# Kernel tuning notes

Measured on AMD Instinct MI355X. Metric: run time of the kernel, lower is better.

Reference implementation:

```python
import jax, jax.numpy as jnp
import numpy as np


def _pairwise_sq_dist_mean(x):
    """Mean over feature dim of pairwise squared distances: D[i,j] = mean_k (x[j,k]-x[i,k])^2.
    Uses the ||a||^2 + ||b||^2 - 2ab identity instead of the O(n^2*d) broadcast."""
    d = x.shape[1]
    sq = jnp.sum(x * x, axis=1)  # [n]
    gram = x @ x.T               # [n, n]
    return (sq[:, None] + sq[None, :] - 2.0 * gram) / d


def setup_inputs() -> dict:
    key = jax.random.key(0)
    k1, k2 = jax.random.split(key)
    noises = jax.random.normal(k1, (4096, 256), dtype=jnp.float32)
    images = jax.random.normal(k2, (4096, 3, 64, 64), dtype=jnp.float32)
    return {"noises": noises, "images": images}


def reference(noises, images):
    if images.ndim > 2:
        images = images.reshape(images.shape[0], -1)
    images_dist = _pairwise_sq_dist_mean(images)  # [B, B]
    noises_dist = _pairwise_sq_dist_mean(noises)  # [B, B]
    return jnp.exp(jnp.mean(-images_dist * noises_dist))
```

## Files before the change

### kernel.cpp

```cpp
#include <hip/hip_runtime.h>
#include <stdint.h>
#include <math.h>

typedef __attribute__((ext_vector_type(8))) short short8;
typedef __attribute__((ext_vector_type(4))) float f32x4;

typedef __attribute__((address_space(1))) const uint32_t g_u32;
typedef __attribute__((address_space(3))) uint32_t l_u32;

static __device__ __forceinline__ uint16_t f2bf(float f) {
  union { float f; uint32_t u; } v; v.f = f;
  uint32_t r = (v.u + 0x7FFFu + ((v.u >> 16) & 1u)) >> 16;
  return (uint16_t)r;
}

static __device__ __forceinline__ float waveReduceSum(float x) {
#pragma unroll
  for (int m = 32; m > 0; m >>= 1) x += __shfl_xor(x, m, 64);
  return x;
}

__global__ __launch_bounds__(256) void k_noise_b(const float* __restrict__ N,
                                                 float* __restrict__ b) {
  const int wave = threadIdx.x >> 6, lane = threadIdx.x & 63;
  const int i = blockIdx.x * 4 + wave;
  const float4 v = *reinterpret_cast<const float4*>(N + (size_t)i * 256 + lane * 4);
  float s = v.x * v.x + v.y * v.y + v.z * v.z + v.w * v.w;
  s = waveReduceSum(s);
  if (lane == 0) b[i] = s;
}

__global__ __launch_bounds__(256) void k_nt(const float* __restrict__ N,
                                            uint16_t* __restrict__ Nt) {
  __shared__ __align__(16) uint16_t T[256 * 72];
  const int i0 = blockIdx.x * 64;
  const int tid = threadIdx.x;
#pragma unroll
  for (int it = 0; it < 16; ++it) {
    const int k = (tid >> 6) + it * 4;
    const int l4 = (tid & 63) * 4;
    const float4 v = *reinterpret_cast<const float4*>(N + (size_t)(i0 + k) * 256 + l4);
    T[(l4 + 0) * 72 + k] = f2bf(v.x);
    T[(l4 + 1) * 72 + k] = f2bf(v.y);
    T[(l4 + 2) * 72 + k] = f2bf(v.z);
    T[(l4 + 3) * 72 + k] = f2bf(v.w);
  }
  __syncthreads();
  const int l = tid;
#pragma unroll
  for (int tt = 0; tt < 2; ++tt) {
    const int tg = blockIdx.x * 2 + tt;
#pragma unroll
    for (int c = 0; c < 4; ++c) {
      const short8 v = *reinterpret_cast<const short8*>(&T[l * 72 + tt * 32 + c * 8]);
      *reinterpret_cast<short8*>((char*)Nt + (size_t)tg * 16384 + l * 64 +
                                 ((c ^ (l & 3)) << 4)) = v;
    }
  }
}

__global__ __launch_bounds__(256) void k_x_pass(const float* __restrict__ X,
                                                const float* __restrict__ b,
                                                float* __restrict__ a,
                                                float* __restrict__ sx,
                                                float* __restrict__ cx, int D1) {
  const int ncb = D1 >> 10;
  const int colblk = blockIdx.x % ncb;
  const int rowblk = blockIdx.x / ncb;
  const int wv = threadIdx.x >> 6, lane = threadIdx.x & 63;
  const int col = (colblk << 10) + (wv << 8) + (lane << 2);
  const int row0 = rowblk << 6;
  float s0 = 0.f, s1 = 0.f, s2 = 0.f, s3 = 0.f;
  float c0 = 0.f, c1 = 0.f, c2 = 0.f, c3 = 0.f;
  const float* p = X + (size_t)row0 * D1 + col;
  for (int r8 = 0; r8 < 64; r8 += 8) {
    float asq[8];
#pragma unroll
    for (int r = 0; r < 8; ++r) {
      const float4 v = *reinterpret_cast<const float4*>(p + (size_t)(r8 + r) * D1);
      const float bi = b[row0 + r8 + r];
      s0 += v.x; s1 += v.y; s2 += v.z; s3 += v.w;
      c0 += bi * v.x; c1 += bi * v.y; c2 += bi * v.z; c3 += bi * v.w;
      asq[r] = v.x * v.x + v.y * v.y + v.z * v.z + v.w * v.w;
    }
#pragma unroll
    for (int m = 1; m < 64; m <<= 1) {
#pragma unroll
      for (int r = 0; r < 8; ++r) asq[r] += __shfl_xor(asq[r], m, 64);
    }
    float myv = asq[0];
#pragma unroll
    for (int r = 1; r < 8; ++r) myv = (lane == r) ? asq[r] : myv;
    if (lane < 8) atomicAdd(&a[row0 + r8 + lane], myv);
  }
  atomicAdd(&sx[col + 0], s0); atomicAdd(&sx[col + 1], s1);
  atomicAdd(&sx[col + 2], s2); atomicAdd(&sx[col + 3], s3);
  atomicAdd(&cx[col + 0], c0); atomicAdd(&cx[col + 1], c1);
  atomicAdd(&cx[col + 2], c2); atomicAdd(&cx[col + 3], c3);
}

__global__ __launch_bounds__(256) void k_noise2(const float* __restrict__ N,
                                                const float* __restrict__ a,
                                                float* __restrict__ sn,
                                                float* __restrict__ an) {
  const int t = threadIdx.x;
  const int i0 = blockIdx.x << 6;
  float ssn = 0.f, san = 0.f;
  for (int r = 0; r < 64; ++r) {
    const int i = i0 + r;
    const float v = N[(size_t)i * 256 + t];
    ssn += v;
    san += a[i] * v;
  }
  atomicAdd(&sn[t], ssn);
  atomicAdd(&an[t], san);
}

__global__ __launch_bounds__(256, 3) void k_gemm_f2(const float* __restrict__ X,
                                                    const uint16_t* __restrict__ Nt,
                                                    float* __restrict__ M,
                                                    int B, int D1) {
  __shared__ __align__(16) uint16_t NB[2][8192];
  __shared__ __align__(16) uint16_t AB[2][64 * 40];
  const int tid = threadIdx.x;
  const int w = tid >> 6, lane = tid & 63;
  const int lr = lane & 15, lh = lane >> 4;
  const int nks = B >> 7;
  const int pt = blockIdx.x >> 2, kc = blockIdx.x & 3;
  const int pbase = pt << 6;
  const int ks0 = kc * nks;

  f32x4 acc[4][4];
#pragma unroll
  for (int i = 0; i < 4; ++i)
#pragma unroll
    for (int j = 0; j < 4; ++j) acc[i][j] = (f32x4){0.f, 0.f, 0.f, 0.f};

  const int ap = tid & 63, ak8 = (tid >> 6) << 3;
  const float* Xbase = X + (size_t)(ks0 * 32 + ak8) * D1 + pbase + ap;
  float xr[8];

#define GLL_B(S, BUF)                                                              \
  {                                                                                \
    const char* gsrc_ = (const char*)Nt + (size_t)(ks0 + (S)) * 16384 +            \
                        ((size_t)w << 10) + (size_t)lane * 16;                     \
    _Pragma("unroll")                                                              \
    for (int j_ = 0; j_ < 4; ++j_) {                                               \
      __builtin_amdgcn_global_load_lds((g_u32*)(gsrc_ + ((size_t)j_ << 12)),       \
                                       (l_u32*)&NB[BUF][(j_ * 4 + w) << 9],        \
                                       16, 0, 0);                                  \
    }                                                                              \
  }
#define A_LOADS(S)                                                                 \
  {                                                                                \
    const float* p_ = Xbase + (size_t)(S) * 32 * D1;                               \
    _Pragma("unroll")                                                              \
    for (int r_ = 0; r_ < 8; ++r_) xr[r_] = p_[(size_t)r_ * D1];                   \
  }

  GLL_B(0, 0);
  A_LOADS(0);

  for (int s = 0; s < nks; ++s) {
    const int buf = s & 1;
    {
      union { uint16_t u[8]; short8 v; } pk;
#pragma unroll
      for (int r = 0; r < 8; ++r) pk.u[r] = f2bf(xr[r]);
      *reinterpret_cast<short8*>(&AB[buf][ap * 40 + ak8]) = pk.v;
    }
    __syncthreads();
    if (s + 1 < nks) {
      GLL_B(s + 1, buf ^ 1);
      A_LOADS(s + 1);
    }
    short8 af[4], bfv[4];
#pragma unroll
    for (int ps = 0; ps < 4; ++ps)
      af[ps] = *reinterpret_cast<const short8*>(&AB[buf][(ps * 16 + lr) * 40 + lh * 8]);
#pragma unroll
    for (int q = 0; q < 4; ++q) {
      const int l = (w << 6) + (q << 4) + lr;
      bfv[q] = *reinterpret_cast<const short8*>(&NB[buf][l * 32 + ((lh ^ (l & 3)) << 3)]);
    }
#pragma unroll
    for (int ps = 0; ps < 4; ++ps)
#pragma unroll
      for (int q = 0; q < 4; ++q)
        acc[ps][q] = __builtin_amdgcn_mfma_f32_16x16x32_bf16(af[ps], bfv[q], acc[ps][q], 0, 0, 0);
    __syncthreads();
  }
#undef GLL_B
#undef A_LOADS

#pragma unroll
  for (int ps = 0; ps < 4; ++ps)
#pragma unroll
    for (int q = 0; q < 4; ++q)
#pragma unroll
      for (int e = 0; e < 4; ++e) {
        const int p = pbase + ps * 16 + lh * 4 + e;
        const int l = (w << 6) + (q << 4) + lr;
        atomicAdd(&M[(size_t)p * 256 + l], acc[ps][q][e]);
      }
}

__global__ __launch_bounds__(256) void k_square(const float* __restrict__ M,
                                                float* __restrict__ Fp, int nf4) {
  __shared__ float red[4];
  float s = 0.f;
  for (int idx = blockIdx.x * 256 + threadIdx.x; idx < nf4; idx += gridDim.x * 256) {
    const float4 v = reinterpret_cast<const float4*>(M)[idx];
    s += v.x * v.x + v.y * v.y + v.z * v.z + v.w * v.w;
  }
  s = waveReduceSum(s);
  const int wave = threadIdx.x >> 6, lane = threadIdx.x & 63;
  if (lane == 0) red[wave] = s;
  __syncthreads();
  if (threadIdx.x == 0) atomicAdd(Fp, red[0] + red[1] + red[2] + red[3]);
}

__global__ __launch_bounds__(256) void k_gemm_f(const float* __restrict__ X,
                                                const float* __restrict__ Nz,
                                                float* __restrict__ Fout,
                                                int B, int D1) {
  __shared__ uint16_t Abf[64 * 40];
  __shared__ uint16_t Bbf[256 * 40];
  __shared__ float red[4];
  const int tid = threadIdx.x;
  const int pbase = blockIdx.x << 6;
  const int wave = tid >> 6, lane = tid & 63;
  const int lr = lane & 15, lh = lane >> 4;

  f32x4 acc[4][4];
#pragma unroll
  for (int i = 0; i < 4; ++i)
#pragma unroll
    for (int j = 0; j < 4; ++j) acc[i][j] = (f32x4){0.f, 0.f, 0.f, 0.f};

  const int igx = tid & 7, p4x = ((tid >> 3) & 15) << 2;
  const int ign0 = tid & 7, l4n0 = (tid >> 3) << 2;
  const int ign1 = (tid + 256) & 7, l4n1 = ((tid + 256) >> 3) << 2;

  float4 xr0, xr1, xr2, xr3;
  float4 n0r0, n0r1, n0r2, n0r3;
  float4 n1r0, n1r1, n1r2, n1r3;

  auto load_stage = [&](int i0) {
    if (tid < 128) {
      const float* src = X + (size_t)(i0 + igx * 4) * D1 + pbase + p4x;
      xr0 = *reinterpret_cast<const float4*>(src);
      xr1 = *reinterpret_cast<const float4*>(src + D1);
      xr2 = *reinterpret_cast<const float4*>(src + 2 * (size_t)D1);
      xr3 = *reinterpret_cast<const float4*>(src + 3 * (size_t)D1);
    }
    {
      const float* src = Nz + (size_t)(i0 + ign0 * 4) * 256 + l4n0;
      n0r0 = *reinterpret_cast<const float4*>(src);
      n0r1 = *reinterpret_cast<const float4*>(src + 256);
      n0r2 = *reinterpret_cast<const float4*>(src + 512);
      n0r3 = *reinterpret_cast<const float4*>(src + 768);
    }
    {
      const float* src = Nz + (size_t)(i0 + ign1 * 4) * 256 + l4n1;
      n1r0 = *reinterpret_cast<const float4*>(src);
      n1r1 = *reinterpret_cast<const float4*>(src + 256);
      n1r2 = *reinterpret_cast<const float4*>(src + 512);
      n1r3 = *reinterpret_cast<const float4*>(src + 768);
    }
  };

  auto store_stage = [&]() {
    ushort4 w;
    if (tid < 128) {
      w.x = f2bf(xr0.x); w.y = f2bf(xr1.x); w.z = f2bf(xr2.x); w.w = f2bf(xr3.x);
      *reinterpret_cast<ushort4*>(&Abf[(p4x + 0) * 40 + igx * 4]) = w;
      w.x = f2bf(xr0.y); w.y = f2bf(xr1.y); w.z = f2bf(xr2.y); w.w = f2bf(xr3.y);
      *reinterpret_cast<ushort4*>(&Abf[(p4x + 1) * 40 + igx * 4]) = w;
      w.x = f2bf(xr0.z); w.y = f2bf(xr1.z); w.z = f2bf(xr2.z); w.w = f2bf(xr3.z);
      *reinterpret_cast<ushort4*>(&Abf[(p4x + 2) * 40 + igx * 4]) = w;
      w.x = f2bf(xr0.w); w.y = f2bf(xr1.w); w.z = f2bf(xr2.w); w.w = f2bf(xr3.w);
      *reinterpret_cast<ushort4*>(&Abf[(p4x + 3) * 40 + igx * 4]) = w;
    }
    w.x = f2bf(n0r0.x); w.y = f2bf(n0r1.x); w.z = f2bf(n0r2.x); w.w = f2bf(n0r3.x);
    *reinterpret_cast<ushort4*>(&Bbf[(l4n0 + 0) * 40 + ign0 * 4]) = w;
    w.x = f2bf(n0r0.y); w.y = f2bf(n0r1.y); w.z = f2bf(n0r2.y); w.w = f2bf(n0r3.y);
    *reinterpret_cast<ushort4*>(&Bbf[(l4n0 + 1) * 40 + ign0 * 4]) = w;
    w.x = f2bf(n0r0.z); w.y = f2bf(n0r1.z); w.z = f2bf(n0r2.z); w.w = f2bf(n0r3.z);
    *reinterpret_cast<ushort4*>(&Bbf[(l4n0 + 2) * 40 + ign0 * 4]) = w;
    w.x = f2bf(n0r0.w); w.y = f2bf(n0r1.w); w.z = f2bf(n0r2.w); w.w = f2bf(n0r3.w);
    *reinterpret_cast<ushort4*>(&Bbf[(l4n0 + 3) * 40 + ign0 * 4]) = w;

    w.x = f2bf(n1r0.x); w.y = f2bf(n1r1.x); w.z = f2bf(n1r2.x); w.w = f2bf(n1r3.x);
    *reinterpret_cast<ushort4*>(&Bbf[(l4n1 + 0) * 40 + ign1 * 4]) = w;
    w.x = f2bf(n1r0.y); w.y = f2bf(n1r1.y); w.z = f2bf(n1r2.y); w.w = f2bf(n1r3.y);
    *reinterpret_cast<ushort4*>(&Bbf[(l4n1 + 1) * 40 + ign1 * 4]) = w;
    w.x = f2bf(n1r0.z); w.y = f2bf(n1r1.z); w.z = f2bf(n1r2.z); w.w = f2bf(n1r3.z);
    *reinterpret_cast<ushort4*>(&Bbf[(l4n1 + 2) * 40 + ign1 * 4]) = w;
    w.x = f2bf(n1r0.w); w.y = f2bf(n1r1.w); w.z = f2bf(n1r2.w); w.w = f2bf(n1r3.w);
    *reinterpret_cast<ushort4*>(&Bbf[(l4n1 + 3) * 40 + ign1 * 4]) = w;
  };

  load_stage(0);
  for (int i0 = 0; i0 < B; i0 += 32) {
    store_stage();
    __syncthreads();
    if (i0 + 32 < B) load_stage(i0 + 32);

    short8 af[4], bfv[4];
#pragma unroll
    for (int ps = 0; ps < 4; ++ps)
      af[ps] = *reinterpret_cast<const short8*>(&Abf[(ps * 16 + lr) * 40 + lh * 8]);
#pragma unroll
    for (int q = 0; q < 4; ++q)
      bfv[q] = *reinterpret_cast<const short8*>(&Bbf[((wave * 4 + q) * 16 + lr) * 40 + lh * 8]);
#pragma unroll
    for (int ps = 0; ps < 4; ++ps)
#pragma unroll
      for (int q = 0; q < 4; ++q)
        acc[ps][q] = __builtin_amdgcn_mfma_f32_16x16x32_bf16(af[ps], bfv[q], acc[ps][q], 0, 0, 0);
    __syncthreads();
  }

  float loc = 0.f;
#pragma unroll
  for (int ps = 0; ps < 4; ++ps)
#pragma unroll
    for (int q = 0; q < 4; ++q)
#pragma unroll
      for (int e = 0; e < 4; ++e) loc += acc[ps][q][e] * acc[ps][q][e];
  loc = waveReduceSum(loc);
  if (lane == 0) red[wave] = loc;
  __syncthreads();
  if (tid == 0) atomicAdd(Fout, red[0] + red[1] + red[2] + red[3]);
}

__global__ __launch_bounds__(256) void k_final(const float* __restrict__ a,
                                               const float* __restrict__ b,
                                               const float* __restrict__ sx,
                                               const float* __restrict__ cx,
                                               const float* __restrict__ sn,
                                               const float* __restrict__ an,
                                               const float* __restrict__ Fp,
                                               float* __restrict__ out, int B, int D1) {
  const int tid = threadIdx.x;
  float sa = 0.f, sb = 0.f, sab = 0.f, t2 = 0.f;
  for (int i = tid; i < B; i += 256) {
    const float ai = a[i], bi = b[i];
    sa += ai; sb += bi; sab += ai * bi;
  }
  float t1 = an[tid] * sn[tid];
  for (int k = tid; k < D1; k += 256) t2 += cx[k] * sx[k];

  sa = waveReduceSum(sa); sb = waveReduceSum(sb); sab = waveReduceSum(sab);
  t1 = waveReduceSum(t1); t2 = waveReduceSum(t2);
  __shared__ float R[5][4];
  const int wave = tid >> 6, lane = tid & 63;
  if (lane == 0) { R[0][wave] = sa; R[1][wave] = sb; R[2][wave] = sab; R[3][wave] = t1; R[4][wave] = t2; }
  __syncthreads();
  if (tid == 0) {
    double Sa = 0, Sb = 0, Sab = 0, T1 = 0, T2 = 0;
    for (int w = 0; w < 4; ++w) {
      Sa += R[0][w]; Sb += R[1][w]; Sab += R[2][w]; T1 += R[3][w]; T2 += R[4][w];
    }
    const double F = (double)Fp[0];
    const double total = 2.0 * (double)B * Sab + 2.0 * Sa * Sb - 4.0 * T1 - 4.0 * T2 + 4.0 * F;
    const double denom = (double)D1 * 256.0 * (double)B * (double)B;
    out[0] = (float)exp(-total / denom);
  }
}

extern "C" void kernel_launch(void* const* d_in, const int* in_sizes, int n_in,
                              void* d_out, int out_size, void* d_ws, size_t ws_size,
                              hipStream_t stream) {
  const float* noises = (const float*)d_in[0];
  const float* images = (const float*)d_in[1];
  const int B = in_sizes[0] / 256;
  const int D1 = in_sizes[1] / B;

  float* ws = (float*)d_ws;
  float* a  = ws;
  float* b  = ws + B;
  float* sx = ws + 2 * B;
  float* cx = ws + 2 * B + D1;
  float* sn = ws + 2 * B + 2 * D1;
  float* an = ws + 2 * B + 2 * D1 + 256;
  float* Fp = ws + 2 * B + 2 * D1 + 512;
  const size_t m_off = 36864;
  float* M  = ws + m_off;
  uint16_t* Nt = (uint16_t*)(ws + m_off + (size_t)D1 * 256);
  float* outf = (float*)d_out;

  const size_t need = (m_off + (size_t)D1 * 256) * sizeof(float) + (size_t)B * 256 * 2;
  const bool big = ws_size >= need;

  if (big) {
    hipMemsetAsync(d_ws, 0, (m_off + (size_t)D1 * 256) * sizeof(float), stream);
    k_noise_b<<<B / 4, 256, 0, stream>>>(noises, b);
    k_nt<<<B / 64, 256, 0, stream>>>(noises, Nt);
    k_x_pass<<<(D1 / 1024) * (B / 64), 256, 0, stream>>>(images, b, a, sx, cx, D1);
    k_noise2<<<B / 64, 256, 0, stream>>>(noises, a, sn, an);
    k_gemm_f2<<<(D1 / 64) * 4, 256, 0, stream>>>(images, Nt, M, B, D1);
    k_square<<<512, 256, 0, stream>>>(M, Fp, D1 * 256 / 4);
    k_final<<<1, 256, 0, stream>>>(a, b, sx, cx, sn, an, Fp, outf, B, D1);
  } else {
    hipMemsetAsync(d_ws, 0, (size_t)(2 * B + 2 * D1 + 513) * sizeof(float), stream);
    k_noise_b<<<B / 4, 256, 0, stream>>>(noises, b);
    k_x_pass<<<(D1 / 1024) * (B / 64), 256, 0, stream>>>(images, b, a, sx, cx, D1);
    k_noise2<<<B / 64, 256, 0, stream>>>(noises, a, sn, an);
    k_gemm_f<<<D1 / 64, 256, 0, stream>>>(images, noises, Fp, B, D1);
    k_final<<<1, 256, 0, stream>>>(a, b, sx, cx, sn, an, Fp, outf, B, D1);
  }
}
```

Before: 177.7 us.

## Fuse image statistics pass into GEMM and store split-K partials as bf16

Drops the separate image-statistics kernel (k_x_pass) and computes the per-column sums, b-weighted sums and the scalar reductions inside the GEMM's A-tile load loop. The noise norms and column sums move into the transpose kernel, and a new small kernel computes h1. Each of the four split-K slices now writes its partial M in bf16 to its own buffer instead of using fp32 atomicAdds, and the square kernel adds the four slices before squaring. The large memset is replaced by a small zero kernel over the accumulators only. This removes a full extra read of the 200MB image tensor and the atomic traffic, at the cost of bf16 rounding on the partial products and more workspace.

```diff
diff --git a/kernel.cpp b/kernel.cpp
--- a/kernel.cpp
+++ b/kernel.cpp
@@ -14,10 +14,258 @@
   return (uint16_t)r;
 }
 
+static __device__ __forceinline__ float bf2f(uint16_t u) {
+  union { uint32_t u; float f; } v; v.u = ((uint32_t)u) << 16;
+  return v.f;
+}
+
 static __device__ __forceinline__ float waveReduceSum(float x) {
 #pragma unroll
   for (int m = 32; m > 0; m >>= 1) x += __shfl_xor(x, m, 64);
   return x;
+}
+
+__global__ __launch_bounds__(256) void k_zero(float* __restrict__ p, int n4) {
+  const int i = blockIdx.x * 256 + threadIdx.x;
+  if (i < n4) reinterpret_cast<float4*>(p)[i] = float4{0.f, 0.f, 0.f, 0.f};
+}
+
+__global__ __launch_bounds__(256) void k_nt(const float* __restrict__ N,
+                                            uint16_t* __restrict__ Nt,
+                                            float* __restrict__ b,
+                                            float* __restrict__ sn) {
+  __shared__ __align__(16) uint16_t T[256 * 72];
+  const int i0 = blockIdx.x * 64;
+  const int tid = threadIdx.x;
+  const int wave = tid >> 6, lane = tid & 63;
+  float sq[16];
+  float snacc0 = 0.f, snacc1 = 0.f, snacc2 = 0.f, snacc3 = 0.f;
+#pragma unroll
+  for (int it = 0; it < 16; ++it) {
+    const int k = wave + it * 4;
+    const int l4 = lane * 4;
+    const float4 v = *reinterpret_cast<const float4*>(N + (size_t)(i0 + k) * 256 + l4);
+    T[(l4 + 0) * 72 + k] = f2bf(v.x);
+    T[(l4 + 1) * 72 + k] = f2bf(v.y);
+    T[(l4 + 2) * 72 + k] = f2bf(v.z);
+    T[(l4 + 3) * 72 + k] = f2bf(v.w);
+    sq[it] = v.x * v.x + v.y * v.y + v.z * v.z + v.w * v.w;
+    snacc0 += v.x; snacc1 += v.y; snacc2 += v.z; snacc3 += v.w;
+  }
+#pragma unroll
+  for (int m = 1; m < 64; m <<= 1) {
+#pragma unroll
+    for (int it = 0; it < 16; ++it) sq[it] += __shfl_xor(sq[it], m, 64);
+  }
+  float myv = sq[0];
+#pragma unroll
+  for (int it = 1; it < 16; ++it) myv = (lane == it) ? sq[it] : myv;
+  if (lane < 16) b[i0 + wave + lane * 4] = myv;
+  {
+    const int l4 = lane * 4;
+    atomicAdd(&sn[l4 + 0], snacc0); atomicAdd(&sn[l4 + 1], snacc1);
+    atomicAdd(&sn[l4 + 2], snacc2); atomicAdd(&sn[l4 + 3], snacc3);
+  }
+  __syncthreads();
+  const int l = tid;
+#pragma unroll
+  for (int tt = 0; tt < 2; ++tt) {
+    const int tg = blockIdx.x * 2 + tt;
+#pragma unroll
+    for (int c = 0; c < 4; ++c) {
+      const short8 v = *reinterpret_cast<const short8*>(&T[l * 72 + tt * 32 + c * 8]);
+      *reinterpret_cast<short8*>((char*)Nt + (size_t)tg * 16384 + l * 64 +
+                                 ((c ^ (l & 3)) << 4)) = v;
+    }
+  }
+}
+
+__global__ __launch_bounds__(256) void k_h1(const float* __restrict__ N,
+                                            const float* __restrict__ sn,
+                                            float* __restrict__ h1) {
+  const int wave = threadIdx.x >> 6, lane = threadIdx.x & 63;
+  const int i = blockIdx.x * 4 + wave;
+  const float4 v = *reinterpret_cast<const float4*>(N + (size_t)i * 256 + lane * 4);
+  const float4 s = *reinterpret_cast<const float4*>(sn + lane * 4);
+  float d = v.x * s.x + v.y * s.y + v.z * s.z + v.w * s.w;
+  d = waveReduceSum(d);
+  if (lane == 0) h1[i] = d;
+}
+
+__global__ __launch_bounds__(256, 3) void k_gemm_f3(const float* __restrict__ X,
+                                                    const uint16_t* __restrict__ Nt,
+                                                    uint16_t* __restrict__ Mb,
+                                                    const float* __restrict__ bvec,
+                                                    const float* __restrict__ h1v,
+                                                    float* __restrict__ sx,
+                                                    float* __restrict__ cx,
+                                                    float* __restrict__ scal,
+                                                    int B, int D1) {
+  __shared__ __align__(16) uint16_t NB[2][8192];
+  __shared__ __align__(16) uint16_t AB[2][64 * 40];
+  __shared__ float SR[3][4];
+  const int tid = threadIdx.x;
+  const int w = tid >> 6, lane = tid & 63;
+  const int lr = lane & 15, lh = lane >> 4;
+  const int nks = B >> 7;
+  const int pt = blockIdx.x >> 2, kc = blockIdx.x & 3;
+  const int pbase = pt << 6;
+  const int ks0 = kc * nks;
+
+  f32x4 acc[4][4];
+#pragma unroll
+  for (int i = 0; i < 4; ++i)
+#pragma unroll
+    for (int j = 0; j < 4; ++j) acc[i][j] = (f32x4){0.f, 0.f, 0.f, 0.f};
+
+  const int ap = tid & 63, ak8 = (tid >> 6) << 3;
+  const float* Xbase = X + (size_t)(ks0 * 32 + ak8) * D1 + pbase + ap;
+  float xr[8];
+  float4 bv0, bv1, hv0, hv1;
+  float s1 = 0.f, sb = 0.f, sh = 0.f, sxa = 0.f, cxa = 0.f;
+
+#define GLL_B(S, BUF)                                                              \
+  {                                                                                \
+    const char* gsrc_ = (const char*)Nt + (size_t)(ks0 + (S)) * 16384 +            \
+                        ((size_t)w << 10) + (size_t)lane * 16;                     \
+    _Pragma("unroll")                                                              \
+    for (int j_ = 0; j_ < 4; ++j_) {                                               \
+      __builtin_amdgcn_global_load_lds((g_u32*)(gsrc_ + ((size_t)j_ << 12)),       \
+                                       (l_u32*)&NB[BUF][(j_ * 4 + w) << 9],        \
+                                       16, 0, 0);                                  \
+    }                                                                              \
+  }
+#define A_LOADS(S)                                                                 \
+  {                                                                                \
+    const float* p_ = Xbase + (size_t)(S) * 32 * D1;                               \
+    _Pragma("unroll")                                                              \
+    for (int r_ = 0; r_ < 8; ++r_) xr[r_] = p_[(size_t)r_ * D1];                   \
+    const int ib_ = ks0 * 32 + (S) * 32 + ak8;                                     \
+    bv0 = *reinterpret_cast<const float4*>(bvec + ib_);                            \
+    bv1 = *reinterpret_cast<const float4*>(bvec + ib_ + 4);                        \
+    hv0 = *reinterpret_cast<const float4*>(h1v + ib_);                             \
+    hv1 = *reinterpret_cast<const float4*>(h1v + ib_ + 4);                         \
+  }
+
+  GLL_B(0, 0);
+  A_LOADS(0);
+
+  for (int s = 0; s < nks; ++s) {
+    const int buf = s & 1;
+    {
+      union { uint16_t u[8]; short8 v; } pk;
+      const float bb[8] = {bv0.x, bv0.y, bv0.z, bv0.w, bv1.x, bv1.y, bv1.z, bv1.w};
+      const float hh[8] = {hv0.x, hv0.y, hv0.z, hv0.w, hv1.x, hv1.y, hv1.z, hv1.w};
+#pragma unroll
+      for (int r = 0; r < 8; ++r) {
+        const float x = xr[r];
+        pk.u[r] = f2bf(x);
+        const float x2 = x * x;
+        s1 += x2;
+        sb += bb[r] * x2;
+        sh += hh[r] * x2;
+        sxa += x;
+        cxa += bb[r] * x;
+      }
+      *reinterpret_cast<short8*>(&AB[buf][ap * 40 + ak8]) = pk.v;
+    }
+    __syncthreads();
+    if (s + 1 < nks) {
+      GLL_B(s + 1, buf ^ 1);
+      A_LOADS(s + 1);
+    }
+    short8 af[4], bfv[4];
+#pragma unroll
+    for (int ps = 0; ps < 4; ++ps)
+      af[ps] = *reinterpret_cast<const short8*>(&AB[buf][(ps * 16 + lr) * 40 + lh * 8]);
+#pragma unroll
+    for (int q = 0; q < 4; ++q) {
+      const int l = (w << 6) + (q << 4) + lr;
+      bfv[q] = *reinterpret_cast<const short8*>(&NB[buf][l * 32 + ((lh ^ (l & 3)) << 3)]);
+    }
+#pragma unroll
+    for (int ps = 0; ps < 4; ++ps)
+#pragma unroll
+      for (int q = 0; q < 4; ++q)
+        acc[ps][q] = __builtin_amdgcn_mfma_f32_16x16x32_bf16(af[ps], bfv[q], acc[ps][q], 0, 0, 0);
+    __syncthreads();
+  }
+#undef GLL_B
+#undef A_LOADS
+
+  uint16_t* Mk = Mb + (size_t)kc * ((size_t)D1 * 256);
+#pragma unroll
+  for (int ps = 0; ps < 4; ++ps)
+#pragma unroll
+    for (int q = 0; q < 4; ++q) {
+      const int l = (w << 6) + (q << 4) + lr;
+      const int p0 = pbase + ps * 16 + lh * 4;
+      ushort4 st;
+      st.x = f2bf(acc[ps][q][0]); st.y = f2bf(acc[ps][q][1]);
+      st.z = f2bf(acc[ps][q][2]); st.w = f2bf(acc[ps][q][3]);
+      *reinterpret_cast<ushort4*>(&Mk[(size_t)l * D1 + p0]) = st;
+    }
+
+  atomicAdd(&sx[pbase + ap], sxa);
+  atomicAdd(&cx[pbase + ap], cxa);
+
+  s1 = waveReduceSum(s1); sb = waveReduceSum(sb); sh = waveReduceSum(sh);
+  if (lane == 0) { SR[0][w] = s1; SR[1][w] = sb; SR[2][w] = sh; }
+  __syncthreads();
+  if (tid == 0) {
+    atomicAdd(&scal[0], SR[0][0] + SR[0][1] + SR[0][2] + SR[0][3]);
+    atomicAdd(&scal[1], SR[1][0] + SR[1][1] + SR[1][2] + SR[1][3]);
+    atomicAdd(&scal[2], SR[2][0] + SR[2][1] + SR[2][2] + SR[2][3]);
+  }
+}
+
+__global__ __launch_bounds__(256) void k_square(const uint16_t* __restrict__ Mb,
+                                                float* __restrict__ Fp,
+                                                int n8, int slice) {
+  __shared__ float red[4];
+  float s = 0.f;
+  for (int idx = blockIdx.x * 256 + threadIdx.x; idx < n8; idx += gridDim.x * 256) {
+    union { short8 v; uint16_t u[8]; } m0, m1, m2, m3;
+    m0.v = *reinterpret_cast<const short8*>(Mb + (size_t)idx * 8);
+    m1.v = *reinterpret_cast<const short8*>(Mb + (size_t)idx * 8 + (size_t)slice);
+    m2.v = *reinterpret_cast<const short8*>(Mb + (size_t)idx * 8 + 2 * (size_t)slice);
+    m3.v = *reinterpret_cast<const short8*>(Mb + (size_t)idx * 8 + 3 * (size_t)slice);
+#pragma unroll
+    for (int e = 0; e < 8; ++e) {
+      const float v = bf2f(m0.u[e]) + bf2f(m1.u[e]) + bf2f(m2.u[e]) + bf2f(m3.u[e]);
+      s += v * v;
+    }
+  }
+  s = waveReduceSum(s);
+  const int wave = threadIdx.x >> 6, lane = threadIdx.x & 63;
+  if (lane == 0) red[wave] = s;
+  __syncthreads();
+  if (threadIdx.x == 0) atomicAdd(Fp, red[0] + red[1] + red[2] + red[3]);
+}
+
+__global__ __launch_bounds__(256) void k_final3(const float* __restrict__ scal,
+                                                const float* __restrict__ b,
+                                                const float* __restrict__ sx,
+                                                const float* __restrict__ cx,
+                                                float* __restrict__ out,
+                                                int B, int D1) {
+  const int tid = threadIdx.x;
+  float sb_ = 0.f, t2_ = 0.f;
+  for (int i = tid; i < B; i += 256) sb_ += b[i];
+  for (int k = tid; k < D1; k += 256) t2_ += sx[k] * cx[k];
+  sb_ = waveReduceSum(sb_); t2_ = waveReduceSum(t2_);
+  __shared__ float R[2][4];
+  const int wave = tid >> 6, lane = tid & 63;
+  if (lane == 0) { R[0][wave] = sb_; R[1][wave] = t2_; }
+  __syncthreads();
+  if (tid == 0) {
+    double Sb = 0, T2 = 0;
+    for (int w = 0; w < 4; ++w) { Sb += R[0][w]; T2 += R[1][w]; }
+    const double Sa = scal[0], Sab = scal[1], T1 = scal[2], F = scal[3];
+    const double total = 2.0 * (double)B * Sab + 2.0 * Sa * Sb - 4.0 * T1 - 4.0 * T2 + 4.0 * F;
+    const double denom = (double)D1 * 256.0 * (double)B * (double)B;
+    out[0] = (float)exp(-total / denom);
+  }
 }
 
 __global__ __launch_bounds__(256) void k_noise_b(const float* __restrict__ N,
@@ -28,35 +276,6 @@
   float s = v.x * v.x + v.y * v.y + v.z * v.z + v.w * v.w;
   s = waveReduceSum(s);
   if (lane == 0) b[i] = s;
-}
-
-__global__ __launch_bounds__(256) void k_nt(const float* __restrict__ N,
-                                            uint16_t* __restrict__ Nt) {
-  __shared__ __align__(16) uint16_t T[256 * 72];
-  const int i0 = blockIdx.x * 64;
-  const int tid = threadIdx.x;
-#pragma unroll
-  for (int it = 0; it < 16; ++it) {
-    const int k = (tid >> 6) + it * 4;
-    const int l4 = (tid & 63) * 4;
-    const float4 v = *reinterpret_cast<const float4*>(N + (size_t)(i0 + k) * 256 + l4);
-    T[(l4 + 0) * 72 + k] = f2bf(v.x);
-    T[(l4 + 1) * 72 + k] = f2bf(v.y);
-    T[(l4 + 2) * 72 + k] = f2bf(v.z);
-    T[(l4 + 3) * 72 + k] = f2bf(v.w);
-  }
-  __syncthreads();
-  const int l = tid;
-#pragma unroll
-  for (int tt = 0; tt < 2; ++tt) {
-    const int tg = blockIdx.x * 2 + tt;
-#pragma unroll
-    for (int c = 0; c < 4; ++c) {
-      const short8 v = *reinterpret_cast<const short8*>(&T[l * 72 + tt * 32 + c * 8]);
-      *reinterpret_cast<short8*>((char*)Nt + (size_t)tg * 16384 + l * 64 +
-                                 ((c ^ (l & 3)) << 4)) = v;
-    }
-  }
 }
 
 __global__ __launch_bounds__(256) void k_x_pass(const float* __restrict__ X,
@@ -116,110 +335,6 @@
   atomicAdd(&an[t], san);
 }
 
-__global__ __launch_bounds__(256, 3) void k_gemm_f2(const float* __restrict__ X,
-                                                    const uint16_t* __restrict__ Nt,
-                                                    float* __restrict__ M,
-                                                    int B, int D1) {
-  __shared__ __align__(16) uint16_t NB[2][8192];
-  __shared__ __align__(16) uint16_t AB[2][64 * 40];
-  const int tid = threadIdx.x;
-  const int w = tid >> 6, lane = tid & 63;
-  const int lr = lane & 15, lh = lane >> 4;
-  const int nks = B >> 7;
-  const int pt = blockIdx.x >> 2, kc = blockIdx.x & 3;
-  const int pbase = pt << 6;
-  const int ks0 = kc * nks;
-
-  f32x4 acc[4][4];
-#pragma unroll
-  for (int i = 0; i < 4; ++i)
-#pragma unroll
-    for (int j = 0; j < 4; ++j) acc[i][j] = (f32x4){0.f, 0.f, 0.f, 0.f};
-
-  const int ap = tid & 63, ak8 = (tid >> 6) << 3;
-  const float* Xbase = X + (size_t)(ks0 * 32 + ak8) * D1 + pbase + ap;
-  float xr[8];
-
-#define GLL_B(S, BUF)                                                              \
-  {                                                                                \
-    const char* gsrc_ = (const char*)Nt + (size_t)(ks0 + (S)) * 16384 +            \
-                        ((size_t)w << 10) + (size_t)lane * 16;                     \
-    _Pragma("unroll")                                                              \
-    for (int j_ = 0; j_ < 4; ++j_) {                                               \
-      __builtin_amdgcn_global_load_lds((g_u32*)(gsrc_ + ((size_t)j_ << 12)),       \
-                                       (l_u32*)&NB[BUF][(j_ * 4 + w) << 9],        \
-                                       16, 0, 0);                                  \
-    }                                                                              \
-  }
-#define A_LOADS(S)                                                                 \
-  {                                                                                \
-    const float* p_ = Xbase + (size_t)(S) * 32 * D1;                               \
-    _Pragma("unroll")                                                              \
-    for (int r_ = 0; r_ < 8; ++r_) xr[r_] = p_[(size_t)r_ * D1];                   \
-  }
-
-  GLL_B(0, 0);
-  A_LOADS(0);
-
-  for (int s = 0; s < nks; ++s) {
-    const int buf = s & 1;
-    {
-      union { uint16_t u[8]; short8 v; } pk;
-#pragma unroll
-      for (int r = 0; r < 8; ++r) pk.u[r] = f2bf(xr[r]);
-      *reinterpret_cast<short8*>(&AB[buf][ap * 40 + ak8]) = pk.v;
-    }
-    __syncthreads();
-    if (s + 1 < nks) {
-      GLL_B(s + 1, buf ^ 1);
-      A_LOADS(s + 1);
-    }
-    short8 af[4], bfv[4];
-#pragma unroll
-    for (int ps = 0; ps < 4; ++ps)
-      af[ps] = *reinterpret_cast<const short8*>(&AB[buf][(ps * 16 + lr) * 40 + lh * 8]);
-#pragma unroll
-    for (int q = 0; q < 4; ++q) {
-      const int l = (w << 6) + (q << 4) + lr;
-      bfv[q] = *reinterpret_cast<const short8*>(&NB[buf][l * 32 + ((lh ^ (l & 3)) << 3)]);
-    }
-#pragma unroll
-    for (int ps = 0; ps < 4; ++ps)
-#pragma unroll
-      for (int q = 0; q < 4; ++q)
-        acc[ps][q] = __builtin_amdgcn_mfma_f32_16x16x32_bf16(af[ps], bfv[q], acc[ps][q], 0, 0, 0);
-    __syncthreads();
-  }
-#undef GLL_B
-#undef A_LOADS
-
-#pragma unroll
-  for (int ps = 0; ps < 4; ++ps)
-#pragma unroll
-    for (int q = 0; q < 4; ++q)
-#pragma unroll
-      for (int e = 0; e < 4; ++e) {
-        const int p = pbase + ps * 16 + lh * 4 + e;
-        const int l = (w << 6) + (q << 4) + lr;
-        atomicAdd(&M[(size_t)p * 256 + l], acc[ps][q][e]);
-      }
-}
-
-__global__ __launch_bounds__(256) void k_square(const float* __restrict__ M,
-                                                float* __restrict__ Fp, int nf4) {
-  __shared__ float red[4];
-  float s = 0.f;
-  for (int idx = blockIdx.x * 256 + threadIdx.x; idx < nf4; idx += gridDim.x * 256) {
-    const float4 v = reinterpret_cast<const float4*>(M)[idx];
-    s += v.x * v.x + v.y * v.y + v.z * v.z + v.w * v.w;
-  }
-  s = waveReduceSum(s);
-  const int wave = threadIdx.x >> 6, lane = threadIdx.x & 63;
-  if (lane == 0) red[wave] = s;
-  __syncthreads();
-  if (threadIdx.x == 0) atomicAdd(Fp, red[0] + red[1] + red[2] + red[3]);
-}
-
 __global__ __launch_bounds__(256) void k_gemm_f(const float* __restrict__ X,
                                                 const float* __restrict__ Nz,
                                                 float* __restrict__ Fout,
@@ -377,38 +492,44 @@
   const float* images = (const float*)d_in[1];
   const int B = in_sizes[0] / 256;
   const int D1 = in_sizes[1] / B;
-
+  float* outf = (float*)d_out;
   float* ws = (float*)d_ws;
-  float* a  = ws;
-  float* b  = ws + B;
-  float* sx = ws + 2 * B;
-  float* cx = ws + 2 * B + D1;
-  float* sn = ws + 2 * B + 2 * D1;
-  float* an = ws + 2 * B + 2 * D1 + 256;
-  float* Fp = ws + 2 * B + 2 * D1 + 512;
-  const size_t m_off = 36864;
-  float* M  = ws + m_off;
-  uint16_t* Nt = (uint16_t*)(ws + m_off + (size_t)D1 * 256);
-  float* outf = (float*)d_out;
-
-  const size_t need = (m_off + (size_t)D1 * 256) * sizeof(float) + (size_t)B * 256 * 2;
-  const bool big = ws_size >= need;
-
-  if (big) {
-    hipMemsetAsync(d_ws, 0, (m_off + (size_t)D1 * 256) * sizeof(float), stream);
-    k_noise_b<<<B / 4, 256, 0, stream>>>(noises, b);
-    k_nt<<<B / 64, 256, 0, stream>>>(noises, Nt);
-    k_x_pass<<<(D1 / 1024) * (B / 64), 256, 0, stream>>>(images, b, a, sx, cx, D1);
-    k_noise2<<<B / 64, 256, 0, stream>>>(noises, a, sn, an);
-    k_gemm_f2<<<(D1 / 64) * 4, 256, 0, stream>>>(images, Nt, M, B, D1);
-    k_square<<<512, 256, 0, stream>>>(M, Fp, D1 * 256 / 4);
-    k_final<<<1, 256, 0, stream>>>(a, b, sx, cx, sn, an, Fp, outf, B, D1);
+
+  float* sx   = ws;
+  float* cx   = ws + D1;
+  float* sn   = ws + 2 * D1;
+  float* scal = ws + 2 * D1 + 256;
+  float* b    = ws + 2 * D1 + 272;
+  float* h1   = b + B;
+  const size_t nt_off_f = (size_t)2 * D1 + 272 + 2 * (size_t)B;
+  const size_t nt_off_a = (nt_off_f + 3) & ~(size_t)3;
+  uint16_t* Nt = (uint16_t*)(ws + nt_off_a);
+  const size_t mb_off_f = nt_off_a + ((size_t)B * 256) / 2;
+  uint16_t* Mb = (uint16_t*)(ws + mb_off_f);
+  const size_t need = (mb_off_f + 2 * (size_t)D1 * 256) * sizeof(float);
+
+  if (ws_size >= need) {
+    const int nzero4 = (2 * D1 + 272) / 4;
+    k_zero<<<(nzero4 + 255) / 256, 256, 0, stream>>>(ws, nzero4);
+    k_nt<<<B / 64, 256, 0, stream>>>(noises, Nt, b, sn);
+    k_h1<<<B / 4, 256, 0, stream>>>(noises, sn, h1);
+    k_gemm_f3<<<(D1 / 64) * 4, 256, 0, stream>>>(images, Nt, Mb, b, h1, sx, cx, scal, B, D1);
+    k_square<<<512, 256, 0, stream>>>(Mb, &scal[3], D1 * 256 / 8, D1 * 256);
+    k_final3<<<1, 256, 0, stream>>>(scal, b, sx, cx, outf, B, D1);
   } else {
-    hipMemsetAsync(d_ws, 0, (size_t)(2 * B + 2 * D1 + 513) * sizeof(float), stream);
-    k_noise_b<<<B / 4, 256, 0, stream>>>(noises, b);
-    k_x_pass<<<(D1 / 1024) * (B / 64), 256, 0, stream>>>(images, b, a, sx, cx, D1);
-    k_noise2<<<B / 64, 256, 0, stream>>>(noises, a, sn, an);
-    k_gemm_f<<<D1 / 64, 256, 0, stream>>>(images, noises, Fp, B, D1);
-    k_final<<<1, 256, 0, stream>>>(a, b, sx, cx, sn, an, Fp, outf, B, D1);
-  }
-}
+    float* a2  = ws;
+    float* b2  = ws + B;
+    float* sx2 = ws + 2 * B;
+    float* cx2 = ws + 2 * B + D1;
+    float* sn2 = ws + 2 * B + 2 * D1;
+    float* an2 = ws + 2 * B + 2 * D1 + 256;
+    float* Fp2 = ws + 2 * B + 2 * D1 + 512;
+    const int nzero4 = (2 * B + 2 * D1 + 516) / 4;
+    k_zero<<<(nzero4 + 255) / 256, 256, 0, stream>>>(ws, nzero4);
+    k_noise_b<<<B / 4, 256, 0, stream>>>(noises, b2);
+    k_x_pass<<<(D1 / 1024) * (B / 64), 256, 0, stream>>>(images, b2, a2, sx2, cx2, D1);
+    k_noise2<<<B / 64, 256, 0, stream>>>(noises, a2, sn2, an2);
+    k_gemm_f<<<D1 / 64, 256, 0, stream>>>(images, noises, Fp2, B, D1);
+    k_final<<<1, 256, 0, stream>>>(a2, b2, sx2, cx2, sn2, an2, Fp2, outf, B, D1);
+  }
+}
```

New measurement: 151.5 us. -14.7%, faster.
